# Performance work log

Hardware: AMD Instinct MI355X
Metric: run time of the kernel (lower is better)

The kernel has to match this reference:

```python
import jax, jax.numpy as jnp
import numpy as np

N, E = 50000, 800000
IN_DIM, HID, ZDIM = 256, 128, 64
LN_EPS = 1e-5


def _layernorm(x, gamma, beta):
    mu = jnp.mean(x, axis=-1, keepdims=True)
    var = jnp.mean(jnp.square(x - mu), axis=-1, keepdims=True)
    return (x - mu) * jax.lax.rsqrt(var + LN_EPS) * gamma + beta


def _gcn_conv(h, src, dst, dinv, W, b):
    # h: (N, d_in) -> (N, d_out). GCNConv: X W, then sym-normalized
    # aggregation over edges with self-loops, then bias.
    h = h @ W                                   # (N, d_out)
    coef = dinv[src] * dinv[dst]                # (E,)
    agg = jax.ops.segment_sum(h[src] * coef[:, None], dst,
                              num_segments=h.shape[0])
    agg = agg + h * jnp.square(dinv)[:, None]   # self-loop term
    return agg + b


def setup_inputs() -> dict:
    key = jax.random.key(0)
    ks = jax.random.split(key, 5)
    x = jax.random.normal(ks[0], (N, IN_DIM), dtype=jnp.float32)
    edge_index = jax.random.randint(ks[1], (2, E), 0, N, dtype=jnp.int64)
    s1 = 1.0 / np.sqrt(IN_DIM)
    s2 = 1.0 / np.sqrt(HID)
    return {
        "x": x,
        "edge_index": edge_index,
        "ln_gamma": jnp.ones((IN_DIM,), jnp.float32),
        "ln_beta": jnp.zeros((IN_DIM,), jnp.float32),
        "W1": jax.random.normal(ks[2], (IN_DIM, HID), jnp.float32) * s1,
        "b1": jnp.zeros((HID,), jnp.float32),
        "W2": jax.random.normal(ks[3], (HID, HID), jnp.float32) * s2,
        "b2": jnp.zeros((HID,), jnp.float32),
        "W3": jax.random.normal(ks[4], (HID, ZDIM), jnp.float32) * s2,
        "b3": jnp.zeros((ZDIM,), jnp.float32),
    }


def reference(x, edge_index, ln_gamma, ln_beta, W1, b1, W2, b2, W3, b3):
    src, dst = edge_index[0], edge_index[1]
    n = x.shape[0]
    # degree with self-loops (dropout is inference no-op, training=False)
    deg = jnp.ones((n,), x.dtype).at[dst].add(1.0)
    dinv = jax.lax.rsqrt(deg)
    h = _layernorm(x, ln_gamma, ln_beta)
    h = jax.nn.relu(_gcn_conv(h, src, dst, dinv, W1, b1))
    h = jax.nn.relu(_gcn_conv(h, src, dst, dinv, W2, b2))
    z = _gcn_conv(h, src, dst, dinv, W3, b3)
    return z
```

## Files before the change

kernel.cpp:

```cpp
#include <hip/hip_runtime.h>
#include <cstdint>
#include <cstddef>


typedef __attribute__((ext_vector_type(8))) __bf16 bf16x8;
typedef __attribute__((ext_vector_type(4))) float f32x4;
typedef _Float16 half_t;
typedef __attribute__((ext_vector_type(8))) _Float16 half8_t;

#define NHIST 256
#define CHUNK 4096
#define MAXB 8192

__global__ __launch_bounds__(256) void prep_misc(
    const int* __restrict__ dst,
    const float* __restrict__ W1, const float* __restrict__ W2,
    const float* __restrict__ W3,
    int* __restrict__ bcnt_multi,
    unsigned short* __restrict__ W1t_hi, unsigned short* __restrict__ W1t_lo,
    unsigned short* __restrict__ W2t_hi, unsigned short* __restrict__ W2t_lo,
    unsigned short* __restrict__ W3t_hi, unsigned short* __restrict__ W3t_lo,
    int E) {
  int blk = blockIdx.x;
  int tid = threadIdx.x;
  if (blk < NHIST) {
    __shared__ int h[256];
    h[tid] = 0;
    __syncthreads();
    for (int e = blk * 256 + tid; e < E; e += NHIST * 256)
      atomicAdd(&h[dst[e] >> 8], 1);
    __syncthreads();
    bcnt_multi[blk * 256 + tid] = h[tid];
    return;
  }
  int idx = (blk - NHIST) * 256 + tid;
  const float* W;
  unsigned short *Th, *Tl;
  int K, NOUT;
  if (idx < 32768) {
    W = W1; Th = W1t_hi; Tl = W1t_lo; K = 256; NOUT = 128;
  } else if (idx < 49152) {
    idx -= 32768;
    W = W2; Th = W2t_hi; Tl = W2t_lo; K = 128; NOUT = 128;
  } else {
    idx -= 49152;
    W = W3; Th = W3t_hi; Tl = W3t_lo; K = 128; NOUT = 64;
  }
  int k = idx / NOUT, c = idx % NOUT;
  float v = W[idx];
  __bf16 h = (__bf16)v;
  __bf16 l = (__bf16)(v - (float)h);
  Th[(size_t)c * K + k] = __builtin_bit_cast(unsigned short, h);
  Tl[(size_t)c * K + k] = __builtin_bit_cast(unsigned short, l);
}

__global__ __launch_bounds__(256) void scan_buckets(const int* __restrict__ bcnt_multi,
                                                    int* __restrict__ bbase,
                                                    int* __restrict__ bcur, int NB, int E) {
  __shared__ int tmp[256];
  int t = threadIdx.x;
  int v = 0;
  for (int h = 0; h < NHIST; ++h) v += bcnt_multi[h * 256 + t];
  tmp[t] = v;
  __syncthreads();
  for (int off = 1; off < 256; off <<= 1) {
    int x = (t >= off) ? tmp[t - off] : 0;
    __syncthreads();
    tmp[t] += x;
    __syncthreads();
  }
  int excl = tmp[t] - v;
  if (t < NB) { bbase[t] = excl; bcur[t] = excl; }
  if (t == 0) bbase[NB] = E;
}

__device__ __forceinline__ void scatter_body(char* smem_raw, int bid,
                                             const int* __restrict__ src,
                                             const int* __restrict__ dst,
                                             int* __restrict__ bcur,
                                             unsigned int* __restrict__ binned, int E) {
  unsigned int* recs = (unsigned int*)smem_raw;
  int* hist = (int*)(smem_raw + 16384);
  int* lbase = hist + 256;
  int* resv = lbase + 256;
  int* cur = resv + 256;
  int t = threadIdx.x;
  int e0 = bid * CHUNK;
  if (e0 >= E) return;
  int len = min(CHUNK, E - e0);
  hist[t] = 0;
  cur[t] = 0;
  __syncthreads();
  for (int i = t; i < len; i += 256) atomicAdd(&hist[dst[e0 + i] >> 8], 1);
  __syncthreads();
  int v = hist[t];
  lbase[t] = v;
  __syncthreads();
  for (int off = 1; off < 256; off <<= 1) {
    int x = (t >= off) ? lbase[t - off] : 0;
    __syncthreads();
    lbase[t] += x;
    __syncthreads();
  }
  int myexcl = lbase[t] - v;
  if (v) resv[t] = atomicAdd(&bcur[t], v);
  __syncthreads();
  lbase[t] = myexcl;
  __syncthreads();
  for (int i = t; i < len; i += 256) {
    int d = dst[e0 + i], s = src[e0 + i];
    int b = d >> 8;
    int r = atomicAdd(&cur[b], 1);
    recs[lbase[b] + r] = ((unsigned int)d << 16) | (unsigned int)s;
  }
  __syncthreads();
  for (int i = t; i < len; i += 256) {
    unsigned int rc = recs[i];
    int b = rc >> 24;
    binned[resv[b] + (i - lbase[b])] = rc;
  }
}

__device__ __forceinline__ void sort_body(char* smem_raw, int b,
                                          const unsigned int* __restrict__ binned,
                                          const int* __restrict__ bbase,
                                          int* __restrict__ srcs,
                                          int* __restrict__ offs,
                                          float* __restrict__ dinv,
                                          int N, int NB, int E) {
  int* sstage = (int*)smem_raw;
  int* hist = (int*)(smem_raw + 32768);
  int* nbase = hist + 256;
  int* cur = nbase + 256;
  int* tmp = cur + 256;
  int t = threadIdx.x;
  int base = bbase[b], end = bbase[b + 1];
  int L = end - base;
  if (L > MAXB) L = MAXB;
  hist[t] = 0;
  __syncthreads();
  for (int i = t; i < L; i += 256)
    atomicAdd(&hist[(binned[base + i] >> 16) & 255], 1);
  __syncthreads();
  int v = hist[t];
  tmp[t] = v;
  __syncthreads();
  for (int off = 1; off < 256; off <<= 1) {
    int x = (t >= off) ? tmp[t - off] : 0;
    __syncthreads();
    tmp[t] += x;
    __syncthreads();
  }
  int excl = tmp[t] - v;
  nbase[t] = excl;
  cur[t] = excl;
  int node = (b << 8) + t;
  if (node < N) {
    offs[node] = base + excl;
    dinv[node] = rsqrtf(1.0f + (float)v);
  }
  if (b == NB - 1 && t == 0) offs[N] = E;
  __syncthreads();
  for (int i = t; i < L; i += 256) {
    unsigned int p = binned[base + i];
    int ld = (p >> 16) & 255;
    int slot = atomicAdd(&cur[ld], 1);
    sstage[slot] = (int)(p & 0xFFFFu);
  }
  __syncthreads();
  for (int i = t; i < L; i += 256) srcs[base + i] = sstage[i];
}

template <int K, int NOUT, bool LN, bool A_FP16>
__device__ __forceinline__ void gemm_body(char* smem_raw, int gbid,
                                          const void* __restrict__ Avoid,
                                          const unsigned short* __restrict__ Wt_hi,
                                          const unsigned short* __restrict__ Wt_lo,
                                          const float* __restrict__ gamma,
                                          const float* __restrict__ beta,
                                          half_t* __restrict__ out, int nrows) {
  constexpr int BM = 64, BK = 32, BKP = BK + 8;
  constexpr int NT = NOUT / 16;
  unsigned short* As_hi = (unsigned short*)smem_raw;
  unsigned short* As_lo = As_hi + BM * BKP;
  unsigned short* Bs_hi = As_lo + BM * BKP;
  unsigned short* Bs_lo = Bs_hi + NOUT * BKP;
  float* mu_s = (float*)(Bs_lo + NOUT * BKP);
  float* rs_s = mu_s + BM;

  const int tid = threadIdx.x;
  const int lane = tid & 63;
  const int w = tid >> 6;
  const int quad = lane >> 4;
  const int l16 = lane & 15;
  const int row0 = gbid * BM;

  if constexpr (LN) {
    const float* A = (const float*)Avoid;
    int r = tid >> 2;
    int part = tid & 3;
    int grow = row0 + r;
    if (grow > nrows - 1) grow = nrows - 1;
    const float4* rp = (const float4*)(A + (size_t)grow * K);
    float s = 0.f, s2 = 0.f;
#pragma unroll
    for (int j = 0; j < K / 16; ++j) {
      float4 v = rp[part * (K / 16) + j];
      s += v.x + v.y + v.z + v.w;
      s2 += v.x * v.x + v.y * v.y + v.z * v.z + v.w * v.w;
    }
    s += __shfl_xor(s, 1);
    s += __shfl_xor(s, 2);
    s2 += __shfl_xor(s2, 1);
    s2 += __shfl_xor(s2, 2);
    if (part == 0) {
      float m = s * (1.0f / (float)K);
      float var = s2 * (1.0f / (float)K) - m * m;
      mu_s[r] = m;
      rs_s[r] = rsqrtf(var + 1e-5f);
    }
    __syncthreads();
  }

  f32x4 acc[NT];
#pragma unroll
  for (int t = 0; t < NT; ++t) acc[t] = (f32x4){0.f, 0.f, 0.f, 0.f};

  for (int k0 = 0; k0 < K; k0 += BK) {
    if constexpr (!A_FP16) {
      const float* A = (const float*)Avoid;
#pragma unroll
      for (int i = 0; i < 2; ++i) {
        int r = i * 32 + (tid >> 3);
        int c4 = (tid & 7) * 4;
        int grow = row0 + r;
        if (grow > nrows - 1) grow = nrows - 1;
        float4 v = *(const float4*)&A[(size_t)grow * K + k0 + c4];
        if constexpr (LN) {
          float m = mu_s[r], s = rs_s[r];
          float4 g = *(const float4*)&gamma[k0 + c4];
          float4 b = *(const float4*)&beta[k0 + c4];
          v.x = (v.x - m) * s * g.x + b.x;
          v.y = (v.y - m) * s * g.y + b.y;
          v.z = (v.z - m) * s * g.z + b.z;
          v.w = (v.w - m) * s * g.w + b.w;
        }
        float vv[4] = {v.x, v.y, v.z, v.w};
#pragma unroll
        for (int j = 0; j < 4; ++j) {
          __bf16 h = (__bf16)vv[j];
          __bf16 l = (__bf16)(vv[j] - (float)h);
          As_hi[r * BKP + c4 + j] = __builtin_bit_cast(unsigned short, h);
          As_lo[r * BKP + c4 + j] = __builtin_bit_cast(unsigned short, l);
        }
      }
    } else {
      const half_t* A = (const half_t*)Avoid;
      int r = tid >> 2;
      int c8 = (tid & 3) * 8;
      int grow = row0 + r;
      if (grow > nrows - 1) grow = nrows - 1;
      half8_t v = *(const half8_t*)&A[(size_t)grow * K + k0 + c8];
#pragma unroll
      for (int j = 0; j < 8; ++j) {
        float f = (float)v[j];
        __bf16 h = (__bf16)f;
        __bf16 l = (__bf16)(f - (float)h);
        As_hi[r * BKP + c8 + j] = __builtin_bit_cast(unsigned short, h);
        As_lo[r * BKP + c8 + j] = __builtin_bit_cast(unsigned short, l);
      }
    }
#pragma unroll
    for (int i = 0; i < NOUT / 64; ++i) {
      int n = i * 64 + (tid >> 2);
      int c8 = (tid & 3) * 8;
      *(uint4*)&Bs_hi[n * BKP + c8] = *(const uint4*)&Wt_hi[(size_t)n * K + k0 + c8];
      *(uint4*)&Bs_lo[n * BKP + c8] = *(const uint4*)&Wt_lo[(size_t)n * K + k0 + c8];
    }
    __syncthreads();

    bf16x8 ah = *(const bf16x8*)&As_hi[(w * 16 + l16) * BKP + quad * 8];
    bf16x8 al = *(const bf16x8*)&As_lo[(w * 16 + l16) * BKP + quad * 8];
#pragma unroll
    for (int t = 0; t < NT; ++t) {
      bf16x8 bh = *(const bf16x8*)&Bs_hi[(t * 16 + l16) * BKP + quad * 8];
      bf16x8 bl = *(const bf16x8*)&Bs_lo[(t * 16 + l16) * BKP + quad * 8];
      acc[t] = __builtin_amdgcn_mfma_f32_16x16x32_bf16(ah, bh, acc[t], 0, 0, 0);
      acc[t] = __builtin_amdgcn_mfma_f32_16x16x32_bf16(al, bh, acc[t], 0, 0, 0);
      acc[t] = __builtin_amdgcn_mfma_f32_16x16x32_bf16(ah, bl, acc[t], 0, 0, 0);
    }
    __syncthreads();
  }

#pragma unroll
  for (int t = 0; t < NT; ++t) {
#pragma unroll
    for (int r = 0; r < 4; ++r) {
      int grow = row0 + w * 16 + quad * 4 + r;
      if (grow < nrows) out[(size_t)grow * NOUT + t * 16 + l16] = (half_t)acc[t][r];
    }
  }
}

__global__ __launch_bounds__(256) void fused_scatter_gemm1(
    const int* __restrict__ src, const int* __restrict__ dst,
    int* __restrict__ bcur, unsigned int* __restrict__ binned, int E,
    const float* __restrict__ x,
    const unsigned short* __restrict__ W1t_hi, const unsigned short* __restrict__ W1t_lo,
    const float* __restrict__ gamma, const float* __restrict__ beta,
    half_t* __restrict__ t, int nrows, int nscat) {
  __shared__ __align__(16) char smem[31232];
  if ((int)blockIdx.x < nscat)
    scatter_body(smem, blockIdx.x, src, dst, bcur, binned, E);
  else
    gemm_body<256, 128, true, false>(smem, blockIdx.x - nscat, x, W1t_hi, W1t_lo,
                                     gamma, beta, t, nrows);
}

__global__ __launch_bounds__(256) void fused_sort_gemm1(
    const unsigned int* __restrict__ binned, const int* __restrict__ bbase,
    int* __restrict__ srcs, int* __restrict__ offs, float* __restrict__ dinv,
    int N, int NB, int E,
    const float* __restrict__ x,
    const unsigned short* __restrict__ W1t_hi, const unsigned short* __restrict__ W1t_lo,
    const float* __restrict__ gamma, const float* __restrict__ beta,
    half_t* __restrict__ t, int nrows, int g1a) {
  __shared__ __align__(16) char smem[36864];
  if ((int)blockIdx.x < NB)
    sort_body(smem, blockIdx.x, binned, bbase, srcs, offs, dinv, N, NB, E);
  else
    gemm_body<256, 128, true, false>(smem, g1a + (blockIdx.x - NB), x, W1t_hi, W1t_lo,
                                     gamma, beta, t, nrows);
}

template <int K, int NOUT>
__launch_bounds__(256)
__global__ void gemm_k(const half_t* __restrict__ A,
                       const unsigned short* __restrict__ Wt_hi,
                       const unsigned short* __restrict__ Wt_lo,
                       half_t* __restrict__ out, int nrows) {
  constexpr int SM = 64 * 40 * 4 + NOUT * 40 * 4 + 512;
  __shared__ __align__(16) char smem[SM];
  gemm_body<K, NOUT, false, true>(smem, blockIdx.x, A, Wt_hi, Wt_lo,
                                  nullptr, nullptr, out, nrows);
}

__global__ __launch_bounds__(256) void agg128_h(const half_t* __restrict__ t,
                                                const int* __restrict__ offs,
                                                const int* __restrict__ srcs,
                                                const float* __restrict__ dinv,
                                                const float* __restrict__ bias,
                                                half_t* __restrict__ out, int n) {
  int gid = blockIdx.x * blockDim.x + threadIdx.x;
  int node = gid >> 6, lane = gid & 63;
  if (node >= n) return;
  int qw = lane >> 4;
  int fl = lane & 15;
  int e0 = offs[node], e1 = offs[node + 1];
  float acc[8] = {0.f, 0.f, 0.f, 0.f, 0.f, 0.f, 0.f, 0.f};
  int e = e0 + qw;
  for (; e + 12 < e1; e += 16) {
    int sa = srcs[e], sb = srcs[e + 4], sc = srcs[e + 8], sd = srcs[e + 12];
    float wa = dinv[sa], wb = dinv[sb], wc = dinv[sc], wd = dinv[sd];
    half8_t va = *(const half8_t*)(t + ((size_t)sa << 7) + fl * 8);
    half8_t vb = *(const half8_t*)(t + ((size_t)sb << 7) + fl * 8);
    half8_t vc = *(const half8_t*)(t + ((size_t)sc << 7) + fl * 8);
    half8_t vd = *(const half8_t*)(t + ((size_t)sd << 7) + fl * 8);
#pragma unroll
    for (int j = 0; j < 8; ++j) {
      acc[j] = fmaf(wa, (float)va[j], acc[j]);
      acc[j] = fmaf(wb, (float)vb[j], acc[j]);
      acc[j] = fmaf(wc, (float)vc[j], acc[j]);
      acc[j] = fmaf(wd, (float)vd[j], acc[j]);
    }
  }
  for (; e < e1; e += 4) {
    int s = srcs[e];
    float w = dinv[s];
    half8_t v = *(const half8_t*)(t + ((size_t)s << 7) + fl * 8);
#pragma unroll
    for (int j = 0; j < 8; ++j) acc[j] = fmaf(w, (float)v[j], acc[j]);
  }
#pragma unroll
  for (int j = 0; j < 8; ++j) {
    acc[j] += __shfl_xor(acc[j], 16);
    acc[j] += __shfl_xor(acc[j], 32);
  }
  if (qw == 0) {
    float di = dinv[node];
    float dii = di * di;
    half8_t sv = *(const half8_t*)(t + ((size_t)node << 7) + fl * 8);
    float4 b0 = *(const float4*)(bias + fl * 8);
    float4 b1 = *(const float4*)(bias + fl * 8 + 4);
    float bb[8] = {b0.x, b0.y, b0.z, b0.w, b1.x, b1.y, b1.z, b1.w};
    half8_t o;
#pragma unroll
    for (int j = 0; j < 8; ++j) {
      float v = di * acc[j] + dii * (float)sv[j] + bb[j];
      o[j] = (half_t)fmaxf(v, 0.f);
    }
    *(half8_t*)(out + ((size_t)node << 7) + fl * 8) = o;
  }
}

__global__ __launch_bounds__(256) void agg64_h(const half_t* __restrict__ t,
                                               const int* __restrict__ offs,
                                               const int* __restrict__ srcs,
                                               const float* __restrict__ dinv,
                                               const float* __restrict__ bias,
                                               float* __restrict__ out, int n) {
  int gid = blockIdx.x * blockDim.x + threadIdx.x;
  int node = gid >> 6, lane = gid & 63;
  if (node >= n) return;
  int og = lane >> 3;
  int fl = lane & 7;
  int e0 = offs[node], e1 = offs[node + 1];
  float acc[8] = {0.f, 0.f, 0.f, 0.f, 0.f, 0.f, 0.f, 0.f};
  int e = e0 + og;
  for (; e + 8 < e1; e += 16) {
    int sa = srcs[e], sb = srcs[e + 8];
    float wa = dinv[sa], wb = dinv[sb];
    half8_t va = *(const half8_t*)(t + ((size_t)sa << 6) + fl * 8);
    half8_t vb = *(const half8_t*)(t + ((size_t)sb << 6) + fl * 8);
#pragma unroll
    for (int j = 0; j < 8; ++j) {
      acc[j] = fmaf(wa, (float)va[j], acc[j]);
      acc[j] = fmaf(wb, (float)vb[j], acc[j]);
    }
  }
  for (; e < e1; e += 8) {
    int s = srcs[e];
    float w = dinv[s];
    half8_t v = *(const half8_t*)(t + ((size_t)s << 6) + fl * 8);
#pragma unroll
    for (int j = 0; j < 8; ++j) acc[j] = fmaf(w, (float)v[j], acc[j]);
  }
#pragma unroll
  for (int j = 0; j < 8; ++j) {
    acc[j] += __shfl_xor(acc[j], 8);
    acc[j] += __shfl_xor(acc[j], 16);
    acc[j] += __shfl_xor(acc[j], 32);
  }
  if (og == 0) {
    float di = dinv[node];
    float dii = di * di;
    half8_t sv = *(const half8_t*)(t + ((size_t)node << 6) + fl * 8);
    float4 b0 = *(const float4*)(bias + fl * 8);
    float4 b1 = *(const float4*)(bias + fl * 8 + 4);
    float bb[8] = {b0.x, b0.y, b0.z, b0.w, b1.x, b1.y, b1.z, b1.w};
    float ov[8];
#pragma unroll
    for (int j = 0; j < 8; ++j) ov[j] = di * acc[j] + dii * (float)sv[j] + bb[j];
    *(float4*)(out + ((size_t)node << 6) + fl * 8) = make_float4(ov[0], ov[1], ov[2], ov[3]);
    *(float4*)(out + ((size_t)node << 6) + fl * 8 + 4) = make_float4(ov[4], ov[5], ov[6], ov[7]);
  }
}

extern "C" void kernel_launch(void* const* d_in, const int* in_sizes, int n_in,
                              void* d_out, int out_size, void* d_ws, size_t ws_size,
                              hipStream_t stream) {
  const float* x = (const float*)d_in[0];
  const int* ei = (const int*)d_in[1];
  const float* gamma = (const float*)d_in[2];
  const float* beta = (const float*)d_in[3];
  const float* W1 = (const float*)d_in[4];
  const float* b1 = (const float*)d_in[5];
  const float* W2 = (const float*)d_in[6];
  const float* b2 = (const float*)d_in[7];
  const float* W3 = (const float*)d_in[8];
  const float* b3 = (const float*)d_in[9];
  float* out = (float*)d_out;

  const int N = in_sizes[0] / 256;
  const int E = in_sizes[1] / 2;
  const int* src = ei;
  const int* dst = ei + E;
  const int NB = (N + 255) >> 8;

  char* ws = (char*)d_ws;
  auto alloc = [&](size_t bytes) -> char* {
    char* p = ws;
    ws += (bytes + 255) & ~(size_t)255;
    return p;
  };
  int* bcnt_multi = (int*)alloc(NHIST * 256 * 4);
  int* bbase = (int*)alloc(257 * 4);
  int* bcur = (int*)alloc(256 * 4);
  unsigned int* binned = (unsigned int*)alloc((size_t)E * 4);
  int* srcs = (int*)alloc((size_t)E * 4);
  int* offs = (int*)alloc((size_t)(N + 1) * 4);
  float* dinv = (float*)alloc((size_t)N * 4);
  half_t* t = (half_t*)alloc((size_t)N * 128 * 2);
  half_t* h = (half_t*)alloc((size_t)N * 128 * 2);
  unsigned short* W1t_hi = (unsigned short*)alloc(256 * 128 * 2);
  unsigned short* W1t_lo = (unsigned short*)alloc(256 * 128 * 2);
  unsigned short* W2t_hi = (unsigned short*)alloc(128 * 128 * 2);
  unsigned short* W2t_lo = (unsigned short*)alloc(128 * 128 * 2);
  unsigned short* W3t_hi = (unsigned short*)alloc(128 * 64 * 2);
  unsigned short* W3t_lo = (unsigned short*)alloc(128 * 64 * 2);

  prep_misc<<<NHIST + 224, 256, 0, stream>>>(
      dst, W1, W2, W3, bcnt_multi, W1t_hi, W1t_lo, W2t_hi, W2t_lo,
      W3t_hi, W3t_lo, E);

  scan_buckets<<<1, 256, 0, stream>>>(bcnt_multi, bbase, bcur, NB, E);

  const int gemm_blocks = (N + 63) / 64;
  const int G1A = gemm_blocks / 2;
  const int G1B = gemm_blocks - G1A;
  const int NSCAT = (E + CHUNK - 1) / CHUNK;
  const int agg_blocks = (N + 3) / 4;

  fused_scatter_gemm1<<<NSCAT + G1A, 256, 0, stream>>>(
      src, dst, bcur, binned, E, x, W1t_hi, W1t_lo, gamma, beta, t, N, NSCAT);

  fused_sort_gemm1<<<NB + G1B, 256, 0, stream>>>(
      binned, bbase, srcs, offs, dinv, N, NB, E, x, W1t_hi, W1t_lo, gamma, beta,
      t, N, G1A);

  agg128_h<<<agg_blocks, 256, 0, stream>>>(t, offs, srcs, dinv, b1, h, N);

  gemm_k<128, 128><<<gemm_blocks, 256, 0, stream>>>(h, W2t_hi, W2t_lo, t, N);
  agg128_h<<<agg_blocks, 256, 0, stream>>>(t, offs, srcs, dinv, b2, h, N);

  gemm_k<128, 64><<<gemm_blocks, 256, 0, stream>>>(h, W3t_hi, W3t_lo, t, N);
  agg64_h<<<agg_blocks, 256, 0, stream>>>(t, offs, srcs, dinv, b3, out, N);
}
```

Baseline: 271.5 us.

## Use fp16 A with split fp16 weights in GEMM2/3 and halve GEMM row tile

For the second and third layer GEMMs, the fp16 activations are now fed directly to fp16 MFMAs. Only the weights are split into a hi part and a lo part scaled by 2048, which cuts the work from three MFMAs per tile to two and drops the per-element bf16 split of A. The GEMM row tile also shrinks from 64 to 32 rows, with the four waves arranged 2x2 over rows and columns, so twice as many blocks run with less shared memory each. The first-layer LN GEMM keeps the bf16 three-product scheme. The fp16 weight-split is less accurate for large values and needs the lo scaling to stay correct.

```diff
diff --git a/kernel.cpp b/kernel.cpp
--- a/kernel.cpp
+++ b/kernel.cpp
@@ -34,12 +34,19 @@
     return;
   }
   int idx = (blk - NHIST) * 256 + tid;
+  if (idx < 32768) {
+    int k = idx / 128, c = idx % 128;
+    float v = W1[idx];
+    __bf16 h = (__bf16)v;
+    __bf16 l = (__bf16)(v - (float)h);
+    W1t_hi[(size_t)c * 256 + k] = __builtin_bit_cast(unsigned short, h);
+    W1t_lo[(size_t)c * 256 + k] = __builtin_bit_cast(unsigned short, l);
+    return;
+  }
   const float* W;
   unsigned short *Th, *Tl;
   int K, NOUT;
-  if (idx < 32768) {
-    W = W1; Th = W1t_hi; Tl = W1t_lo; K = 256; NOUT = 128;
-  } else if (idx < 49152) {
+  if (idx < 49152) {
     idx -= 32768;
     W = W2; Th = W2t_hi; Tl = W2t_lo; K = 128; NOUT = 128;
   } else {
@@ -48,8 +55,8 @@
   }
   int k = idx / NOUT, c = idx % NOUT;
   float v = W[idx];
-  __bf16 h = (__bf16)v;
-  __bf16 l = (__bf16)(v - (float)h);
+  half_t h = (half_t)v;
+  half_t l = (half_t)((v - (float)h) * 2048.0f);
   Th[(size_t)c * K + k] = __builtin_bit_cast(unsigned short, h);
   Tl[(size_t)c * K + k] = __builtin_bit_cast(unsigned short, l);
 }
@@ -179,59 +186,62 @@
                                           const float* __restrict__ gamma,
                                           const float* __restrict__ beta,
                                           half_t* __restrict__ out, int nrows) {
-  constexpr int BM = 64, BK = 32, BKP = BK + 8;
-  constexpr int NT = NOUT / 16;
-  unsigned short* As_hi = (unsigned short*)smem_raw;
-  unsigned short* As_lo = As_hi + BM * BKP;
-  unsigned short* Bs_hi = As_lo + BM * BKP;
-  unsigned short* Bs_lo = Bs_hi + NOUT * BKP;
-  float* mu_s = (float*)(Bs_lo + NOUT * BKP);
-  float* rs_s = mu_s + BM;
+  constexpr int BM = 32, BK = 32, BKP = BK + 8;
+  constexpr int NTW = NOUT / 32;
 
   const int tid = threadIdx.x;
   const int lane = tid & 63;
   const int w = tid >> 6;
   const int quad = lane >> 4;
   const int l16 = lane & 15;
+  const int rg = (w & 1) * 16;
+  const int cg = (w >> 1) * (NOUT / 2);
   const int row0 = gbid * BM;
 
-  if constexpr (LN) {
+  if constexpr (!A_FP16) {
+    unsigned short* As_hi = (unsigned short*)smem_raw;
+    unsigned short* As_lo = As_hi + BM * BKP;
+    unsigned short* Bs_hi = As_lo + BM * BKP;
+    unsigned short* Bs_lo = Bs_hi + NOUT * BKP;
+    float* mu_s = (float*)(Bs_lo + NOUT * BKP);
+    float* rs_s = mu_s + BM;
     const float* A = (const float*)Avoid;
-    int r = tid >> 2;
-    int part = tid & 3;
-    int grow = row0 + r;
-    if (grow > nrows - 1) grow = nrows - 1;
-    const float4* rp = (const float4*)(A + (size_t)grow * K);
-    float s = 0.f, s2 = 0.f;
-#pragma unroll
-    for (int j = 0; j < K / 16; ++j) {
-      float4 v = rp[part * (K / 16) + j];
-      s += v.x + v.y + v.z + v.w;
-      s2 += v.x * v.x + v.y * v.y + v.z * v.z + v.w * v.w;
-    }
-    s += __shfl_xor(s, 1);
-    s += __shfl_xor(s, 2);
-    s2 += __shfl_xor(s2, 1);
-    s2 += __shfl_xor(s2, 2);
-    if (part == 0) {
-      float m = s * (1.0f / (float)K);
-      float var = s2 * (1.0f / (float)K) - m * m;
-      mu_s[r] = m;
-      rs_s[r] = rsqrtf(var + 1e-5f);
-    }
-    __syncthreads();
-  }
-
-  f32x4 acc[NT];
-#pragma unroll
-  for (int t = 0; t < NT; ++t) acc[t] = (f32x4){0.f, 0.f, 0.f, 0.f};
-
-  for (int k0 = 0; k0 < K; k0 += BK) {
-    if constexpr (!A_FP16) {
-      const float* A = (const float*)Avoid;
-#pragma unroll
-      for (int i = 0; i < 2; ++i) {
-        int r = i * 32 + (tid >> 3);
+
+    if constexpr (LN) {
+      int r = tid >> 3;
+      int part = tid & 7;
+      int grow = row0 + r;
+      if (grow > nrows - 1) grow = nrows - 1;
+      const float4* rp = (const float4*)(A + (size_t)grow * K);
+      float s = 0.f, s2 = 0.f;
+#pragma unroll
+      for (int j = 0; j < K / 32; ++j) {
+        float4 v = rp[part * (K / 32) + j];
+        s += v.x + v.y + v.z + v.w;
+        s2 += v.x * v.x + v.y * v.y + v.z * v.z + v.w * v.w;
+      }
+      s += __shfl_xor(s, 1);
+      s += __shfl_xor(s, 2);
+      s += __shfl_xor(s, 4);
+      s2 += __shfl_xor(s2, 1);
+      s2 += __shfl_xor(s2, 2);
+      s2 += __shfl_xor(s2, 4);
+      if (part == 0) {
+        float m = s * (1.0f / (float)K);
+        float var = s2 * (1.0f / (float)K) - m * m;
+        mu_s[r] = m;
+        rs_s[r] = rsqrtf(var + 1e-5f);
+      }
+      __syncthreads();
+    }
+
+    f32x4 acc[NTW];
+#pragma unroll
+    for (int t = 0; t < NTW; ++t) acc[t] = (f32x4){0.f, 0.f, 0.f, 0.f};
+
+    for (int k0 = 0; k0 < K; k0 += BK) {
+      {
+        int r = tid >> 3;
         int c4 = (tid & 7) * 4;
         int grow = row0 + r;
         if (grow > nrows - 1) grow = nrows - 1;
@@ -254,54 +264,94 @@
           As_lo[r * BKP + c4 + j] = __builtin_bit_cast(unsigned short, l);
         }
       }
-    } else {
-      const half_t* A = (const half_t*)Avoid;
-      int r = tid >> 2;
-      int c8 = (tid & 3) * 8;
-      int grow = row0 + r;
-      if (grow > nrows - 1) grow = nrows - 1;
-      half8_t v = *(const half8_t*)&A[(size_t)grow * K + k0 + c8];
-#pragma unroll
-      for (int j = 0; j < 8; ++j) {
-        float f = (float)v[j];
-        __bf16 h = (__bf16)f;
-        __bf16 l = (__bf16)(f - (float)h);
-        As_hi[r * BKP + c8 + j] = __builtin_bit_cast(unsigned short, h);
-        As_lo[r * BKP + c8 + j] = __builtin_bit_cast(unsigned short, l);
-      }
-    }
-#pragma unroll
-    for (int i = 0; i < NOUT / 64; ++i) {
-      int n = i * 64 + (tid >> 2);
-      int c8 = (tid & 3) * 8;
-      *(uint4*)&Bs_hi[n * BKP + c8] = *(const uint4*)&Wt_hi[(size_t)n * K + k0 + c8];
-      *(uint4*)&Bs_lo[n * BKP + c8] = *(const uint4*)&Wt_lo[(size_t)n * K + k0 + c8];
-    }
-    __syncthreads();
-
-    bf16x8 ah = *(const bf16x8*)&As_hi[(w * 16 + l16) * BKP + quad * 8];
-    bf16x8 al = *(const bf16x8*)&As_lo[(w * 16 + l16) * BKP + quad * 8];
-#pragma unroll
-    for (int t = 0; t < NT; ++t) {
-      bf16x8 bh = *(const bf16x8*)&Bs_hi[(t * 16 + l16) * BKP + quad * 8];
-      bf16x8 bl = *(const bf16x8*)&Bs_lo[(t * 16 + l16) * BKP + quad * 8];
-      acc[t] = __builtin_amdgcn_mfma_f32_16x16x32_bf16(ah, bh, acc[t], 0, 0, 0);
-      acc[t] = __builtin_amdgcn_mfma_f32_16x16x32_bf16(al, bh, acc[t], 0, 0, 0);
-      acc[t] = __builtin_amdgcn_mfma_f32_16x16x32_bf16(ah, bl, acc[t], 0, 0, 0);
-    }
-    __syncthreads();
-  }
-
-#pragma unroll
-  for (int t = 0; t < NT; ++t) {
-#pragma unroll
-    for (int r = 0; r < 4; ++r) {
-      int grow = row0 + w * 16 + quad * 4 + r;
-      if (grow < nrows) out[(size_t)grow * NOUT + t * 16 + l16] = (half_t)acc[t][r];
-    }
-  }
-}
-
+#pragma unroll
+      for (int i = 0; i < NOUT / 64; ++i) {
+        int n = i * 64 + (tid >> 2);
+        int c8 = (tid & 3) * 8;
+        *(uint4*)&Bs_hi[n * BKP + c8] = *(const uint4*)&Wt_hi[(size_t)n * K + k0 + c8];
+        *(uint4*)&Bs_lo[n * BKP + c8] = *(const uint4*)&Wt_lo[(size_t)n * K + k0 + c8];
+      }
+      __syncthreads();
+
+      bf16x8 ah = *(const bf16x8*)&As_hi[(rg + l16) * BKP + quad * 8];
+      bf16x8 al = *(const bf16x8*)&As_lo[(rg + l16) * BKP + quad * 8];
+#pragma unroll
+      for (int t = 0; t < NTW; ++t) {
+        bf16x8 bh = *(const bf16x8*)&Bs_hi[(cg + t * 16 + l16) * BKP + quad * 8];
+        bf16x8 bl = *(const bf16x8*)&Bs_lo[(cg + t * 16 + l16) * BKP + quad * 8];
+        acc[t] = __builtin_amdgcn_mfma_f32_16x16x32_bf16(ah, bh, acc[t], 0, 0, 0);
+        acc[t] = __builtin_amdgcn_mfma_f32_16x16x32_bf16(al, bh, acc[t], 0, 0, 0);
+        acc[t] = __builtin_amdgcn_mfma_f32_16x16x32_bf16(ah, bl, acc[t], 0, 0, 0);
+      }
+      __syncthreads();
+    }
+
+#pragma unroll
+    for (int t = 0; t < NTW; ++t) {
+#pragma unroll
+      for (int r = 0; r < 4; ++r) {
+        int grow = row0 + rg + quad * 4 + r;
+        if (grow < nrows)
+          out[(size_t)grow * NOUT + cg + t * 16 + l16] = (half_t)acc[t][r];
+      }
+    }
+  } else {
+    half_t* As = (half_t*)smem_raw;
+    half_t* Bs_hi = As + BM * BKP;
+    half_t* Bs_lo = Bs_hi + NOUT * BKP;
+    const half_t* A = (const half_t*)Avoid;
+
+    f32x4 acc1[NTW], acc2[NTW];
+#pragma unroll
+    for (int t = 0; t < NTW; ++t) {
+      acc1[t] = (f32x4){0.f, 0.f, 0.f, 0.f};
+      acc2[t] = (f32x4){0.f, 0.f, 0.f, 0.f};
+    }
+
+    for (int k0 = 0; k0 < K; k0 += BK) {
+      {
+        int r = tid >> 3;
+        int c4 = (tid & 7) * 4;
+        int grow = row0 + r;
+        if (grow > nrows - 1) grow = nrows - 1;
+        *(uint2*)&As[r * BKP + c4] = *(const uint2*)&A[(size_t)grow * K + k0 + c4];
+      }
+#pragma unroll
+      for (int i = 0; i < NOUT / 64; ++i) {
+        int n = i * 64 + (tid >> 2);
+        int c8 = (tid & 3) * 8;
+        *(uint4*)&Bs_hi[n * BKP + c8] =
+            *(const uint4*)&Wt_hi[(size_t)n * K + k0 + c8];
+        *(uint4*)&Bs_lo[n * BKP + c8] =
+            *(const uint4*)&Wt_lo[(size_t)n * K + k0 + c8];
+      }
+      __syncthreads();
+
+      half8_t av = *(const half8_t*)&As[(rg + l16) * BKP + quad * 8];
+#pragma unroll
+      for (int t = 0; t < NTW; ++t) {
+        half8_t bh = *(const half8_t*)&Bs_hi[(cg + t * 16 + l16) * BKP + quad * 8];
+        half8_t bl = *(const half8_t*)&Bs_lo[(cg + t * 16 + l16) * BKP + quad * 8];
+        acc1[t] = __builtin_amdgcn_mfma_f32_16x16x32_f16(av, bh, acc1[t], 0, 0, 0);
+        acc2[t] = __builtin_amdgcn_mfma_f32_16x16x32_f16(av, bl, acc2[t], 0, 0, 0);
+      }
+      __syncthreads();
+    }
+
+#pragma unroll
+    for (int t = 0; t < NTW; ++t) {
+#pragma unroll
+      for (int r = 0; r < 4; ++r) {
+        int grow = row0 + rg + quad * 4 + r;
+        if (grow < nrows)
+          out[(size_t)grow * NOUT + cg + t * 16 + l16] =
+              (half_t)(acc1[t][r] + acc2[t][r] * (1.0f / 2048.0f));
+      }
+    }
+  }
+}
+
+constexpr int GEMM1_SMEM = 32 * 40 * 4 + 128 * 40 * 4 + 256;
 __global__ __launch_bounds__(256) void fused_scatter_gemm1(
     const int* __restrict__ src, const int* __restrict__ dst,
     int* __restrict__ bcur, unsigned int* __restrict__ binned, int E,
@@ -309,7 +359,7 @@
     const unsigned short* __restrict__ W1t_hi, const unsigned short* __restrict__ W1t_lo,
     const float* __restrict__ gamma, const float* __restrict__ beta,
     half_t* __restrict__ t, int nrows, int nscat) {
-  __shared__ __align__(16) char smem[31232];
+  __shared__ __align__(16) char smem[GEMM1_SMEM];
   if ((int)blockIdx.x < nscat)
     scatter_body(smem, blockIdx.x, src, dst, bcur, binned, E);
   else
@@ -339,7 +389,7 @@
                        const unsigned short* __restrict__ Wt_hi,
                        const unsigned short* __restrict__ Wt_lo,
                        half_t* __restrict__ out, int nrows) {
-  constexpr int SM = 64 * 40 * 4 + NOUT * 40 * 4 + 512;
+  constexpr int SM = 32 * 40 * 2 + NOUT * 40 * 4;
   __shared__ __align__(16) char smem[SM];
   gemm_body<K, NOUT, false, true>(smem, blockIdx.x, A, Wt_hi, Wt_lo,
                                   nullptr, nullptr, out, nrows);
@@ -505,7 +555,7 @@
 
   scan_buckets<<<1, 256, 0, stream>>>(bcnt_multi, bbase, bcur, NB, E);
 
-  const int gemm_blocks = (N + 63) / 64;
+  const int gemm_blocks = (N + 31) / 32;
   const int G1A = gemm_blocks / 2;
   const int G1B = gemm_blocks - G1A;
   const int NSCAT = (E + CHUNK - 1) / CHUNK;
```

Result: no change. 268.7 us (-1.0%).
